# Kernel tuning notes

Hardware: AMD Instinct MI355X
Metric: run time of the kernel (lower is better)

Reference implementation:

```python
import jax, jax.numpy as jnp
import numpy as np

B, M, E, NPOS, F, NHEAD, NLAYERS, DFF = 32, 512, 512, 1024, 768, 8, 2, 2048
S = M + 1

def _pe(embed, pad):
    pos = np.arange(pad, dtype=np.float32)[:, None]
    i = np.arange(embed)[None, :]
    ang = pos / np.power(10000.0, (i // 2 * 2.0) / embed)
    pe = np.where(i % 2 == 0, np.sin(ang), np.cos(ang))
    return jnp.asarray(pe, jnp.float32)

PE = _pe(E, M)  # [M, E] sinusoidal table, matches pos_embedding()

def _ln(x, w, b, eps=1e-5):
    mu = x.mean(-1, keepdims=True)
    var = ((x - mu) ** 2).mean(-1, keepdims=True)
    return (x - mu) / jnp.sqrt(var + eps) * w + b

def _mha(x, wi, bi, wo, bo):
    # x: [L, N, E] where L is the attended axis (torch seq dim)
    L, N, Em = x.shape
    Dh = Em // NHEAD
    q, k, v = jnp.split(x @ wi.T + bi, 3, axis=-1)
    q = q.reshape(L, N, NHEAD, Dh) * np.float32(1.0 / np.sqrt(Dh))
    k = k.reshape(L, N, NHEAD, Dh)
    v = v.reshape(L, N, NHEAD, Dh)
    att = jax.nn.softmax(jnp.einsum('lnhd,mnhd->nhlm', q, k), axis=-1)
    o = jnp.einsum('nhlm,mnhd->lnhd', att, v).reshape(L, N, Em)
    return o @ wo.T + bo

def _encoder(x, enc):
    wi, bi, wo, bo, ln1w, ln1b, ln2w, ln2b, w1, b1, w2, b2 = enc
    for l in range(NLAYERS):  # post-norm TransformerEncoderLayer, ReLU, eval mode
        x = _ln(x + _mha(x, wi[l], bi[l], wo[l], bo[l]), ln1w[l], ln1b[l])
        h = jax.nn.relu(x @ w1[l].T + b1[l]) @ w2[l].T + b2[l]
        x = _ln(x + h, ln2w[l], ln2b[l])
    return x

def _forward(pos1, pos2, bert_feature, final_base, emb_table, enc, w_model, w_disc, b_disc):
    emb_table = emb_table.at[0].set(0.0)  # padding_idx=0
    embed = emb_table[pos2] + PE          # [B, M, E]
    starts, ends = pos1[..., 0], pos1[..., 1]
    # loop breaks at first span with end==0: valid = prefix of nonzero ends
    valid = jnp.cumprod((ends != 0).astype(jnp.int32), axis=1).astype(bool)
    k = jnp.arange(M)
    cover = valid[:, :, None] & (starts[:, :, None] <= k) & (k < ends[:, :, None])  # [B, Mspan, Mpos]
    # later spans overwrite earlier ones -> take max covering span index
    span_id = jnp.max(jnp.where(cover, jnp.arange(M)[None, :, None], -1), axis=1)  # [B, Mpos]
    filled = jnp.take_along_axis(embed, jnp.clip(span_id, 0, M - 1)[..., None], axis=1)
    final = jnp.where(span_id[..., None] >= 0, filled, final_base)  # [B, M, E]
    cls = jnp.broadcast_to(emb_table[1], (B, 1, E))
    x = jnp.concatenate([cls, final], axis=1)  # [B, S, E]; torch encoder treats dim0 as seq
    x = _encoder(x, enc)
    pos_feature = jnp.tanh(x @ w_model.T)      # [B, S, F]
    z = jnp.concatenate([bert_feature, pos_feature], axis=-1) @ w_disc.T + b_disc
    return jax.nn.sigmoid(z)                   # [B, S, 1]

def setup_inputs():
    key = jax.random.key(0)
    ks = jax.random.split(key, 12)
    sc = 0.02
    n_valid, chunk = 120, 4  # contiguous spans [4j, 4j+4) for j < 120, then end==0 terminator
    j = np.arange(M)
    starts = np.where(j < n_valid, j * chunk, 0)
    ends = np.where(j < n_valid, j * chunk + chunk, 0)
    pos1 = np.broadcast_to(np.stack([starts, ends], -1), (B, M, 2)).astype(np.int32)
    return {
        'pos1': jnp.asarray(pos1),
        'pos2': jax.random.randint(ks[0], (B, M), 2, NPOS),
        'bert_feature': jax.random.normal(ks[1], (B, S, F), jnp.float32),
        'final_base': jax.random.uniform(ks[2], (B, M, E), jnp.float32),
        'emb_table': jax.random.normal(ks[3], (NPOS, E), jnp.float32) * sc,
        'enc_in_proj_w': jax.random.normal(ks[4], (NLAYERS, 3 * E, E), jnp.float32) * sc,
        'enc_in_proj_b': jnp.zeros((NLAYERS, 3 * E), jnp.float32),
        'enc_out_proj_w': jax.random.normal(ks[5], (NLAYERS, E, E), jnp.float32) * sc,
        'enc_out_proj_b': jnp.zeros((NLAYERS, E), jnp.float32),
        'enc_ln1_w': jnp.ones((NLAYERS, E), jnp.float32),
        'enc_ln1_b': jnp.zeros((NLAYERS, E), jnp.float32),
        'enc_ln2_w': jnp.ones((NLAYERS, E), jnp.float32),
        'enc_ln2_b': jnp.zeros((NLAYERS, E), jnp.float32),
        'enc_ffn_w1': jax.random.normal(ks[6], (NLAYERS, DFF, E), jnp.float32) * sc,
        'enc_ffn_b1': jnp.zeros((NLAYERS, DFF), jnp.float32),
        'enc_ffn_w2': jax.random.normal(ks[7], (NLAYERS, E, DFF), jnp.float32) * sc,
        'enc_ffn_b2': jnp.zeros((NLAYERS, E), jnp.float32),
        'w_model': jax.random.normal(ks[8], (F, E), jnp.float32) * sc,
        'w_disc': jax.random.normal(ks[9], (1, 2 * F), jnp.float32) * sc,
        'b_disc': jnp.zeros((1,), jnp.float32),
    }

def reference(pos1, pos2, bert_feature, final_base, emb_table,
              enc_in_proj_w, enc_in_proj_b, enc_out_proj_w, enc_out_proj_b,
              enc_ln1_w, enc_ln1_b, enc_ln2_w, enc_ln2_b,
              enc_ffn_w1, enc_ffn_b1, enc_ffn_w2, enc_ffn_b2,
              w_model, w_disc, b_disc):
    enc = (enc_in_proj_w, enc_in_proj_b, enc_out_proj_w, enc_out_proj_b,
           enc_ln1_w, enc_ln1_b, enc_ln2_w, enc_ln2_b,
           enc_ffn_w1, enc_ffn_b1, enc_ffn_w2, enc_ffn_b2)
    return _forward(pos1, pos2, bert_feature, final_base, emb_table, enc, w_model, w_disc, b_disc)
```

## Files before the change

kernel.cpp:

```cpp
#include <hip/hip_runtime.h>
#include <hip/hip_bf16.h>

#define B_   32
#define M_   512
#define E_   512
#define S_   513
#define T_   (B_ * S_)
#define TP_  16512
#define NH_  8
#define DH_  64
#define F_   768
#define DFF_ 2048

#define GMT_ 129

typedef short short8 __attribute__((ext_vector_type(8)));
typedef float floatx4 __attribute__((ext_vector_type(4)));

__device__ __forceinline__ float bf2f(unsigned short u) {
    return __uint_as_float(((unsigned int)u) << 16);
}
__device__ __forceinline__ unsigned short f2b_rne(float f) {
    unsigned int u = __float_as_uint(f);
    unsigned int r = u + 0x7FFF + ((u >> 16) & 1);
    return (unsigned short)(r >> 16);
}
__device__ __forceinline__ void gload16(const void* g, void* l) {
    __builtin_amdgcn_global_load_lds(
        (const __attribute__((address_space(1))) void*)g,
        (__attribute__((address_space(3))) void*)l, 16, 0, 0);
}
__device__ __forceinline__ void wait_vm0() { __builtin_amdgcn_s_waitcnt(0x0F70); }

__global__ void span_kernel(const int* __restrict__ pos1, int* __restrict__ span) {
    int b = blockIdx.x;
    __shared__ int st[M_], en[M_];
    __shared__ int redm[4];
    int tid = threadIdx.x;
    for (int j = tid; j < M_; j += 256) {
        st[j] = pos1[(b * M_ + j) * 2];
        en[j] = pos1[(b * M_ + j) * 2 + 1];
    }
    __syncthreads();
    int idx = M_;
    for (int j = tid; j < M_; j += 256)
        if (en[j] == 0 && j < idx) idx = j;
    for (int off = 32; off; off >>= 1) idx = min(idx, __shfl_down(idx, off));
    if ((tid & 63) == 0) redm[tid >> 6] = idx;
    __syncthreads();
    int n = min(min(redm[0], redm[1]), min(redm[2], redm[3]));
    for (int k = tid; k < M_; k += 256) {
        int best = -1;
        for (int j = 0; j < n; ++j)
            if (st[j] <= k && k < en[j]) best = j;
        span[b * M_ + k] = best;
    }
}

__global__ void f2b5_kernel(const float* __restrict__ s0, const float* __restrict__ s1,
                            const float* __restrict__ s2, const float* __restrict__ s3,
                            const float* __restrict__ s4,
                            unsigned short* __restrict__ dst,
                            int c0, int c1, int c2, int c3, int c4) {
    int i = (blockIdx.x * 256 + threadIdx.x) * 4;
    if (i >= c4) return;
    const float* src;
    if      (i < c0) src = s0 + i;
    else if (i < c1) src = s1 + (i - c0);
    else if (i < c2) src = s2 + (i - c1);
    else if (i < c3) src = s3 + (i - c2);
    else             src = s4 + (i - c3);
    float4 v = *(const float4*)src;
    ushort4 o;
    o.x = f2b_rne(v.x); o.y = f2b_rne(v.y); o.z = f2b_rne(v.z); o.w = f2b_rne(v.w);
    *(ushort4*)&dst[i] = o;
}

__global__ __launch_bounds__(256) void build_x(const float* __restrict__ emb,
                        const int* __restrict__ pos2,
                        const float* __restrict__ fbase,
                        const int* __restrict__ span,
                        float* __restrict__ x,
                        unsigned short* __restrict__ xb) {
    int gid = blockIdx.x * 256 + threadIdx.x;
    int t  = gid >> 6;
    int e0 = (gid & 63) * 8;
    int s = t % S_;
    int b = t / S_;
    float v[8];
    if (s == 0) {
        float4 a = *(const float4*)&emb[E_ + e0];
        float4 c = *(const float4*)&emb[E_ + e0 + 4];
        v[0]=a.x; v[1]=a.y; v[2]=a.z; v[3]=a.w; v[4]=c.x; v[5]=c.y; v[6]=c.z; v[7]=c.w;
    } else {
        int k = s - 1;
        int sid = span[b * M_ + k];
        if (sid >= 0) {
            int p = pos2[b * M_ + sid];
            const float* er = emb + (size_t)p * E_ + e0;
            float4 a = *(const float4*)er;
            float4 c = *(const float4*)(er + 4);
            v[0]=a.x; v[1]=a.y; v[2]=a.z; v[3]=a.w; v[4]=c.x; v[5]=c.y; v[6]=c.z; v[7]=c.w;
            float fs = (float)sid;
#pragma unroll
            for (int jj = 0; jj < 4; ++jj) {
                float ex = (float)(e0 + 2 * jj) * (1.0f / 512.0f);
                float ang = fs * exp2f(-ex * 13.287712379549449f);
                float sn, cs;
                __sincosf(ang, &sn, &cs);
                v[2 * jj]     += sn;
                v[2 * jj + 1] += cs;
            }
        } else {
            const float* fr = fbase + ((size_t)b * M_ + k) * E_ + e0;
            float4 a = *(const float4*)fr;
            float4 c = *(const float4*)(fr + 4);
            v[0]=a.x; v[1]=a.y; v[2]=a.z; v[3]=a.w; v[4]=c.x; v[5]=c.y; v[6]=c.z; v[7]=c.w;
        }
    }
    size_t o = (size_t)t * E_ + e0;
    *(float4*)&x[o]     = make_float4(v[0], v[1], v[2], v[3]);
    *(float4*)&x[o + 4] = make_float4(v[4], v[5], v[6], v[7]);
    short8 ob;
#pragma unroll
    for (int j = 0; j < 8; ++j) ob[j] = (short)f2b_rne(v[j]);
    *(short8*)&xb[o] = ob;
}

template <int ACT, int KT>
__global__ __launch_bounds__(256, 4) void gemm_bf16(const unsigned short* __restrict__ A,
                                                    const unsigned short* __restrict__ W,
                                                    const float* __restrict__ bias,
                                                    unsigned short* __restrict__ Cb,
                                                    int T, int O,
                                                    const float* __restrict__ wdz,
                                                    float* __restrict__ zout) {
    constexpr int K = KT;
    constexpr int NSTEP = K / 32;
    __shared__ __align__(16) unsigned short sA[2][128 * 32];
    __shared__ __align__(16) unsigned short sB[2][128 * 32];
    int tid = threadIdx.x;
    int lane = tid & 63, wv = tid >> 6;
    int wr = (wv >> 1) * 64, wc = (wv & 1) * 64;

    int gn = O / 128;
    int per_panel = 8 * gn;
    int id = blockIdx.x;
    int p = id / per_panel;
    int r = id - p * per_panel;
    int mrem = GMT_ - p * 8; if (mrem > 8) mrem = 8;
    int mt = p * 8 + r % mrem;
    int nt = r / mrem;
    int t0 = mt * 128, o0 = nt * 128;

    floatx4 acc[4][4] = {};

    const unsigned short* Ag = A + (size_t)(t0 + wv * 32 + (lane >> 2)) * K + (lane & 3) * 8;
    const unsigned short* Bg = W + (size_t)(o0 + wv * 32 + (lane >> 2)) * K + (lane & 3) * 8;
    const size_t row16 = (size_t)16 * K;
    unsigned short* dA0 = &sA[0][wv * 1024];
    unsigned short* dB0 = &sB[0][wv * 1024];

    int fr = lane & 15;
    int fk = (lane >> 4) * 8;

    gload16(Ag, dA0);
    gload16(Ag + row16, dA0 + 512);
    gload16(Bg, dB0);
    gload16(Bg + row16, dB0 + 512);
    wait_vm0();
    __syncthreads();

#pragma unroll 2
    for (int s = 0; s < NSTEP; ++s) {
        const int cur = s & 1;
        if (s + 1 < NSTEP) {
            const int k = (s + 1) * 32;
            unsigned short* dA = &sA[cur ^ 1][wv * 1024];
            unsigned short* dB = &sB[cur ^ 1][wv * 1024];
            gload16(Ag + k, dA);
            gload16(Ag + row16 + k, dA + 512);
            gload16(Bg + k, dB);
            gload16(Bg + row16 + k, dB + 512);
        }

        short8 af[4], bfr[4];
#pragma unroll
        for (int i = 0; i < 4; ++i)
            af[i] = *(const short8*)&sA[cur][(wr + i * 16 + fr) * 32 + fk];
#pragma unroll
        for (int j = 0; j < 4; ++j)
            bfr[j] = *(const short8*)&sB[cur][(wc + j * 16 + fr) * 32 + fk];
#pragma unroll
        for (int i = 0; i < 4; ++i)
#pragma unroll
            for (int j = 0; j < 4; ++j)
                acc[i][j] = __builtin_amdgcn_mfma_f32_16x16x32_bf16(af[i], bfr[j], acc[i][j], 0, 0, 0);

        wait_vm0();
        __syncthreads();
    }

    int cr = (lane >> 4) * 4;
    int cc = lane & 15;
    if (ACT == 2) {
        float zp[4][4];
#pragma unroll
        for (int i = 0; i < 4; ++i)
#pragma unroll
            for (int rr = 0; rr < 4; ++rr) zp[i][rr] = 0.f;
#pragma unroll
        for (int j = 0; j < 4; ++j) {
            int gn_ = o0 + wc + j * 16 + cc;
            float wz = wdz[gn_];
#pragma unroll
            for (int i = 0; i < 4; ++i)
#pragma unroll
                for (int rr = 0; rr < 4; ++rr)
                    zp[i][rr] += tanhf(acc[i][j][rr]) * wz;
        }
#pragma unroll
        for (int i = 0; i < 4; ++i)
#pragma unroll
            for (int rr = 0; rr < 4; ++rr) {
                float v = zp[i][rr];
                v += __shfl_xor(v, 1);
                v += __shfl_xor(v, 2);
                v += __shfl_xor(v, 4);
                v += __shfl_xor(v, 8);
                if (cc == 0) {
                    int gm_ = t0 + wr + i * 16 + cr + rr;
                    if (gm_ < T) atomicAdd(&zout[gm_], v);
                }
            }
        return;
    }
#pragma unroll
    for (int i = 0; i < 4; ++i) {
#pragma unroll
        for (int j = 0; j < 4; ++j) {
            int gn_ = o0 + wc + j * 16 + cc;
            float bv = bias ? bias[gn_] : 0.f;
#pragma unroll
            for (int rr = 0; rr < 4; ++rr) {
                int gm_ = t0 + wr + i * 16 + cr + rr;
                if (gm_ >= T) continue;
                float v = acc[i][j][rr] + bv;
                if (ACT == 1) v = fmaxf(v, 0.f);
                Cb[(size_t)gm_ * O + gn_] = f2b_rne(v);
            }
        }
    }
}

__global__ __launch_bounds__(64) void attn_mfma(const unsigned short* __restrict__ qkv,
                                                unsigned short* __restrict__ o) {
    __shared__ __align__(16) unsigned short vt[64 * 40];
    __shared__ __align__(16) unsigned short ps[32 * 40];
    int s = blockIdx.x, h = blockIdx.y;
    int lane = threadIdx.x;
    int hd = h * 64;
    int fr = lane & 15, fq = lane >> 4;

    {
        int m = lane >> 1;
        int d0 = (lane & 1) * 32;
        const unsigned short* vrow = qkv + ((size_t)m * S_ + s) * 1536 + 1024 + hd + d0;
        short8 v0 = *(const short8*)(vrow);
        short8 v1 = *(const short8*)(vrow + 8);
        short8 v2 = *(const short8*)(vrow + 16);
        short8 v3 = *(const short8*)(vrow + 24);
#pragma unroll
        for (int j = 0; j < 8; ++j) {
            vt[(d0 + j) * 40 + m]      = (unsigned short)v0[j];
            vt[(d0 + 8 + j) * 40 + m]  = (unsigned short)v1[j];
            vt[(d0 + 16 + j) * 40 + m] = (unsigned short)v2[j];
            vt[(d0 + 24 + j) * 40 + m] = (unsigned short)v3[j];
        }
    }

    floatx4 c[2][2] = {};
#pragma unroll
    for (int ks = 0; ks < 2; ++ks) {
        short8 aq[2], bk[2];
#pragma unroll
        for (int lt = 0; lt < 2; ++lt) {
            int l = lt * 16 + fr;
            aq[lt] = *(const short8*)(qkv + ((size_t)l * S_ + s) * 1536 + hd + ks * 32 + fq * 8);
        }
#pragma unroll
        for (int mt = 0; mt < 2; ++mt) {
            int m = mt * 16 + fr;
            bk[mt] = *(const short8*)(qkv + ((size_t)m * S_ + s) * 1536 + 512 + hd + ks * 32 + fq * 8);
        }
#pragma unroll
        for (int lt = 0; lt < 2; ++lt)
#pragma unroll
            for (int mt = 0; mt < 2; ++mt)
                c[lt][mt] = __builtin_amdgcn_mfma_f32_16x16x32_bf16(aq[lt], bk[mt], c[lt][mt], 0, 0, 0);
    }

#pragma unroll
    for (int lt = 0; lt < 2; ++lt) {
#pragma unroll
        for (int r = 0; r < 4; ++r) {
            float a = c[lt][0][r] * 0.125f;
            float b = c[lt][1][r] * 0.125f;
            float mx = fmaxf(a, b);
#pragma unroll
            for (int off = 1; off < 16; off <<= 1) mx = fmaxf(mx, __shfl_xor(mx, off));
            float ea = expf(a - mx), eb = expf(b - mx);
            float sm = ea + eb;
#pragma unroll
            for (int off = 1; off < 16; off <<= 1) sm += __shfl_xor(sm, off);
            float inv = 1.f / sm;
            int l = lt * 16 + fq * 4 + r;
            ps[l * 40 + fr]      = f2b_rne(ea * inv);
            ps[l * 40 + 16 + fr] = f2b_rne(eb * inv);
        }
    }
    __syncthreads();

    short8 pa[2], vb[4];
#pragma unroll
    for (int lt = 0; lt < 2; ++lt)
        pa[lt] = *(const short8*)&ps[(lt * 16 + fr) * 40 + fq * 8];
#pragma unroll
    for (int dt = 0; dt < 4; ++dt)
        vb[dt] = *(const short8*)&vt[(dt * 16 + fr) * 40 + fq * 8];

    floatx4 oa[2][4] = {};
#pragma unroll
    for (int lt = 0; lt < 2; ++lt)
#pragma unroll
        for (int dt = 0; dt < 4; ++dt)
            oa[lt][dt] = __builtin_amdgcn_mfma_f32_16x16x32_bf16(pa[lt], vb[dt], oa[lt][dt], 0, 0, 0);

#pragma unroll
    for (int lt = 0; lt < 2; ++lt)
#pragma unroll
        for (int dt = 0; dt < 4; ++dt)
#pragma unroll
            for (int r = 0; r < 4; ++r) {
                int l = lt * 16 + fq * 4 + r;
                o[((size_t)l * S_ + s) * E_ + hd + dt * 16 + fr] = f2b_rne(oa[lt][dt][r]);
            }
}

__global__ __launch_bounds__(256) void add_ln(float* __restrict__ x,
                                              unsigned short* __restrict__ xb,
                                              const unsigned short* __restrict__ h,
                                              const float* __restrict__ w,
                                              const float* __restrict__ b) {
    int t = (blockIdx.x << 2) + (threadIdx.x >> 6);
    int lane = threadIdx.x & 63;
    int i0 = lane * 8;
    float* xr = x + (size_t)t * E_;
    const unsigned short* hr = h + (size_t)t * E_;
    float4 xv0 = *(const float4*)&xr[i0];
    float4 xv1 = *(const float4*)&xr[i0 + 4];
    short8 hv = *(const short8*)&hr[i0];
    float v[8];
    v[0] = xv0.x + bf2f((unsigned short)hv[0]);
    v[1] = xv0.y + bf2f((unsigned short)hv[1]);
    v[2] = xv0.z + bf2f((unsigned short)hv[2]);
    v[3] = xv0.w + bf2f((unsigned short)hv[3]);
    v[4] = xv1.x + bf2f((unsigned short)hv[4]);
    v[5] = xv1.y + bf2f((unsigned short)hv[5]);
    v[6] = xv1.z + bf2f((unsigned short)hv[6]);
    v[7] = xv1.w + bf2f((unsigned short)hv[7]);

    float sum = 0.f;
#pragma unroll
    for (int j = 0; j < 8; ++j) sum += v[j];
#pragma unroll
    for (int off = 32; off; off >>= 1) sum += __shfl_xor(sum, off);
    float mu = sum * (1.0f / E_);

    float qs = 0.f;
#pragma unroll
    for (int j = 0; j < 8; ++j) { float d = v[j] - mu; qs += d * d; }
#pragma unroll
    for (int off = 32; off; off >>= 1) qs += __shfl_xor(qs, off);
    float rstd = rsqrtf(qs * (1.0f / E_) + 1e-5f);

    float4 wv0 = *(const float4*)&w[i0];
    float4 wv1 = *(const float4*)&w[i0 + 4];
    float4 bv0 = *(const float4*)&b[i0];
    float4 bv1 = *(const float4*)&b[i0 + 4];
    float o[8];
    o[0] = (v[0] - mu) * rstd * wv0.x + bv0.x;
    o[1] = (v[1] - mu) * rstd * wv0.y + bv0.y;
    o[2] = (v[2] - mu) * rstd * wv0.z + bv0.z;
    o[3] = (v[3] - mu) * rstd * wv0.w + bv0.w;
    o[4] = (v[4] - mu) * rstd * wv1.x + bv1.x;
    o[5] = (v[5] - mu) * rstd * wv1.y + bv1.y;
    o[6] = (v[6] - mu) * rstd * wv1.z + bv1.z;
    o[7] = (v[7] - mu) * rstd * wv1.w + bv1.w;
    *(float4*)&xr[i0]     = make_float4(o[0], o[1], o[2], o[3]);
    *(float4*)&xr[i0 + 4] = make_float4(o[4], o[5], o[6], o[7]);
    short8 ob;
#pragma unroll
    for (int j = 0; j < 8; ++j) ob[j] = (short)f2b_rne(o[j]);
    *(short8*)&xb[(size_t)t * E_ + i0] = ob;
}

__global__ __launch_bounds__(256) void disc_kernel(const float* __restrict__ bert,
                                                   const float* __restrict__ z,
                                                   const float* __restrict__ wd,
                                                   const float* __restrict__ bd,
                                                   float* __restrict__ out) {
    int t = (blockIdx.x << 2) + (threadIdx.x >> 6);
    int lane = threadIdx.x & 63;
    int i0 = lane * 12;
    const float* br = bert + (size_t)t * F_ + i0;
    const float* wr = wd + i0;
    float s = 0.f;
#pragma unroll
    for (int j = 0; j < 12; j += 4) {
        float4 bv = *(const float4*)(br + j);
        float4 wv = *(const float4*)(wr + j);
        s += bv.x * wv.x + bv.y * wv.y + bv.z * wv.z + bv.w * wv.w;
    }
#pragma unroll
    for (int off = 32; off; off >>= 1) s += __shfl_xor(s, off);
    if (lane == 0) {
        float zz = s + z[t] + bd[0];
        out[t] = 1.f / (1.f + expf(-zz));
    }
}

extern "C" void kernel_launch(void* const* d_in, const int* in_sizes, int n_in,
                              void* d_out, int out_size, void* d_ws, size_t ws_size,
                              hipStream_t stream) {
    const int*   pos1 = (const int*)d_in[0];
    const int*   pos2 = (const int*)d_in[1];
    const float* bert = (const float*)d_in[2];
    const float* fb   = (const float*)d_in[3];
    const float* emb  = (const float*)d_in[4];
    const float* wi   = (const float*)d_in[5];
    const float* bi   = (const float*)d_in[6];
    const float* wo   = (const float*)d_in[7];
    const float* bo   = (const float*)d_in[8];
    const float* ln1w = (const float*)d_in[9];
    const float* ln1b = (const float*)d_in[10];
    const float* ln2w = (const float*)d_in[11];
    const float* ln2b = (const float*)d_in[12];
    const float* w1   = (const float*)d_in[13];
    const float* b1   = (const float*)d_in[14];
    const float* w2   = (const float*)d_in[15];
    const float* b2   = (const float*)d_in[16];
    const float* wm   = (const float*)d_in[17];
    const float* wd   = (const float*)d_in[18];
    const float* bd   = (const float*)d_in[19];
    float* out = (float*)d_out;

    float* ws   = (float*)d_ws;
    int*   span = (int*)ws;
    float* x    = ws + 16384;
    unsigned short* xb  = (unsigned short*)(x + (size_t)T_ * 512);
    unsigned short* atb = xb + (size_t)TP_ * 512;
    unsigned short* hb  = atb + (size_t)TP_ * 512;
    unsigned short* U   = hb + (size_t)T_ * 512;
    unsigned short* qkvb = U;
    unsigned short* h1b  = U;
    unsigned short* wib  = U + (size_t)TP_ * 2048;
    const int NWI = 2 * 1536 * 512;
    const int NWO = 2 * 512 * 512;
    const int NW1 = 2 * 2048 * 512;
    const int NW2 = 2 * 512 * 2048;
    const int NWM = 768 * 512;
    unsigned short* wob = wib + NWI;
    unsigned short* w1b = wob + NWO;
    unsigned short* w2b = w1b + NW1;
    unsigned short* wmb = w2b + NW2;
    float* z = (float*)atb;

    span_kernel<<<B_, 256, 0, stream>>>(pos1, span);
    {
        int c0 = NWI, c1 = c0 + NWO, c2 = c1 + NW1, c3 = c2 + NW2, c4 = c3 + NWM;
        f2b5_kernel<<<(c4 / 4 + 255) / 256, 256, 0, stream>>>(wi, wo, w1, w2, wm, wib,
                                                              c0, c1, c2, c3, c4);
    }
    build_x<<<T_ / 4, 256, 0, stream>>>(emb, pos2, fb, span, x, xb);

    for (int l = 0; l < 2; ++l) {
        gemm_bf16<0, 512><<<GMT_ * (1536 / 128), 256, 0, stream>>>(
            xb, wib + (size_t)l * 1536 * 512, bi + l * 1536, qkvb, T_, 1536, nullptr, nullptr);
        attn_mfma<<<dim3(S_, NH_), 64, 0, stream>>>(qkvb, atb);
        gemm_bf16<0, 512><<<GMT_ * (512 / 128), 256, 0, stream>>>(
            atb, wob + (size_t)l * 512 * 512, bo + l * 512, hb, T_, 512, nullptr, nullptr);
        add_ln<<<T_ / 4, 256, 0, stream>>>(x, xb, hb, ln1w + l * 512, ln1b + l * 512);
        gemm_bf16<1, 512><<<GMT_ * (2048 / 128), 256, 0, stream>>>(
            xb, w1b + (size_t)l * 2048 * 512, b1 + l * 2048, h1b, T_, 2048, nullptr, nullptr);
        gemm_bf16<0, 2048><<<GMT_ * (512 / 128), 256, 0, stream>>>(
            h1b, w2b + (size_t)l * 512 * 2048, b2 + l * 512, hb, T_, 512, nullptr, nullptr);
        add_ln<<<T_ / 4, 256, 0, stream>>>(x, xb, hb, ln2w + l * 512, ln2b + l * 512);
    }
    hipMemsetAsync(z, 0, (size_t)T_ * sizeof(float), stream);
    gemm_bf16<2, 512><<<GMT_ * (768 / 128), 256, 0, stream>>>(
        xb, wmb, nullptr, nullptr, T_, 768, wd + F_, z);
    disc_kernel<<<T_ / 4, 256, 0, stream>>>(bert, z, wd, bd, out);
}
```

Before: 740.7 us.

## Triple-buffer GEMM LDS tiles with swizzled layout and deeper prefetch

The bf16 GEMM moves from double to triple buffering in LDS, so loads for step t+2 are issued while step t computes. It waits with a partial vmcnt and a single barrier per step instead of draining all loads. It also XOR-swizzles the 16-byte chunk position within each row to reduce LDS bank conflicts on fragment reads, and raises MFMA issue priority with s_setprio. The larger LDS footprint lowers the occupancy hint from 4 to 3 blocks per CU.

```diff
diff --git a/kernel.cpp b/kernel.cpp
--- a/kernel.cpp
+++ b/kernel.cpp
@@ -30,7 +30,6 @@
         (const __attribute__((address_space(1))) void*)g,
         (__attribute__((address_space(3))) void*)l, 16, 0, 0);
 }
-__device__ __forceinline__ void wait_vm0() { __builtin_amdgcn_s_waitcnt(0x0F70); }
 
 __global__ void span_kernel(const int* __restrict__ pos1, int* __restrict__ span) {
     int b = blockIdx.x;
@@ -128,7 +127,7 @@
 }
 
 template <int ACT, int KT>
-__global__ __launch_bounds__(256, 4) void gemm_bf16(const unsigned short* __restrict__ A,
+__global__ __launch_bounds__(256, 3) void gemm_bf16(const unsigned short* __restrict__ A,
                                                     const unsigned short* __restrict__ W,
                                                     const float* __restrict__ bias,
                                                     unsigned short* __restrict__ Cb,
@@ -137,8 +136,8 @@
                                                     float* __restrict__ zout) {
     constexpr int K = KT;
     constexpr int NSTEP = K / 32;
-    __shared__ __align__(16) unsigned short sA[2][128 * 32];
-    __shared__ __align__(16) unsigned short sB[2][128 * 32];
+    __shared__ __align__(16) unsigned short sA[3][128 * 32];
+    __shared__ __align__(16) unsigned short sB[3][128 * 32];
     int tid = threadIdx.x;
     int lane = tid & 63, wv = tid >> 6;
     int wr = (wv >> 1) * 64, wc = (wv & 1) * 64;
@@ -155,51 +154,63 @@
 
     floatx4 acc[4][4] = {};
 
-    const unsigned short* Ag = A + (size_t)(t0 + wv * 32 + (lane >> 2)) * K + (lane & 3) * 8;
-    const unsigned short* Bg = W + (size_t)(o0 + wv * 32 + (lane >> 2)) * K + (lane & 3) * 8;
+    int swz_st = (((lane & 3) ^ ((lane >> 3) & 3))) * 8;
+    const unsigned short* Ag = A + (size_t)(t0 + wv * 32 + (lane >> 2)) * K + swz_st;
+    const unsigned short* Bg = W + (size_t)(o0 + wv * 32 + (lane >> 2)) * K + swz_st;
     const size_t row16 = (size_t)16 * K;
-    unsigned short* dA0 = &sA[0][wv * 1024];
-    unsigned short* dB0 = &sB[0][wv * 1024];
+    const int wvo = wv * 1024;
 
     int fr = lane & 15;
-    int fk = (lane >> 4) * 8;
-
-    gload16(Ag, dA0);
-    gload16(Ag + row16, dA0 + 512);
-    gload16(Bg, dB0);
-    gload16(Bg + row16, dB0 + 512);
-    wait_vm0();
-    __syncthreads();
-
-#pragma unroll 2
-    for (int s = 0; s < NSTEP; ++s) {
-        const int cur = s & 1;
-        if (s + 1 < NSTEP) {
-            const int k = (s + 1) * 32;
-            unsigned short* dA = &sA[cur ^ 1][wv * 1024];
-            unsigned short* dB = &sB[cur ^ 1][wv * 1024];
-            gload16(Ag + k, dA);
-            gload16(Ag + row16 + k, dA + 512);
-            gload16(Bg + k, dB);
-            gload16(Bg + row16 + k, dB + 512);
-        }
-
+    int fks = (((lane >> 4) ^ ((lane >> 1) & 3))) * 8;
+
+    auto stage = [&](unsigned short* da, unsigned short* db, int k) {
+        gload16(Ag + k, da + wvo);
+        gload16(Ag + row16 + k, da + wvo + 512);
+        gload16(Bg + k, db + wvo);
+        gload16(Bg + row16 + k, db + wvo + 512);
+    };
+    auto compute = [&](const unsigned short* ca, const unsigned short* cb) {
         short8 af[4], bfr[4];
 #pragma unroll
         for (int i = 0; i < 4; ++i)
-            af[i] = *(const short8*)&sA[cur][(wr + i * 16 + fr) * 32 + fk];
+            af[i] = *(const short8*)&ca[(wr + i * 16 + fr) * 32 + fks];
 #pragma unroll
         for (int j = 0; j < 4; ++j)
-            bfr[j] = *(const short8*)&sB[cur][(wc + j * 16 + fr) * 32 + fk];
+            bfr[j] = *(const short8*)&cb[(wc + j * 16 + fr) * 32 + fks];
+        __builtin_amdgcn_s_setprio(1);
 #pragma unroll
         for (int i = 0; i < 4; ++i)
 #pragma unroll
             for (int j = 0; j < 4; ++j)
                 acc[i][j] = __builtin_amdgcn_mfma_f32_16x16x32_bf16(af[i], bfr[j], acc[i][j], 0, 0, 0);
-
-        wait_vm0();
-        __syncthreads();
-    }
+        __builtin_amdgcn_s_setprio(0);
+    };
+
+    unsigned short *a0 = sA[0], *a1 = sA[1], *a2 = sA[2];
+    unsigned short *b0 = sB[0], *b1 = sB[1], *b2 = sB[2];
+
+    stage(a0, b0, 0);
+    stage(a1, b1, 32);
+
+#pragma unroll 3
+    for (int t = 0; t < NSTEP - 2; ++t) {
+        asm volatile("s_waitcnt vmcnt(4)" ::: "memory");
+        __builtin_amdgcn_s_barrier();
+        asm volatile("" ::: "memory");
+        stage(a2, b2, (t + 2) * 32);
+        compute(a0, b0);
+        unsigned short* ta = a0; a0 = a1; a1 = a2; a2 = ta;
+        unsigned short* tb = b0; b0 = b1; b1 = b2; b2 = tb;
+    }
+    asm volatile("s_waitcnt vmcnt(4)" ::: "memory");
+    __builtin_amdgcn_s_barrier();
+    asm volatile("" ::: "memory");
+    compute(a0, b0);
+    a0 = a1; b0 = b1;
+    asm volatile("s_waitcnt vmcnt(0)" ::: "memory");
+    __builtin_amdgcn_s_barrier();
+    asm volatile("" ::: "memory");
+    compute(a0, b0);
 
     int cr = (lane >> 4) * 4;
     int cc = lane & 15;
```

New measurement: 732.9 us. About the same (-1.1%).
